# Performance work log

Measured on AMD Instinct MI355X. Metric: run time of the kernel, lower is better.

## Reference

```python
import jax, jax.numpy as jnp
import numpy as np

B, T, D, H, L = 2, 2048, 1024, 16, 12
DH = D // H


def setup_inputs() -> dict:
    key = jax.random.key(0)
    ks = jax.random.split(key, 12)
    s = 1.0 / np.sqrt(D)
    inp = {
        "x": jax.random.normal(ks[0], (B, T, D), dtype=jnp.float32),
        "Wq": jax.random.normal(ks[1], (D, D), dtype=jnp.float32) * s,
        "bq": jnp.zeros((D,), jnp.float32),
        "Wk": jax.random.normal(ks[2], (D, D), dtype=jnp.float32) * s,
        "bk": jnp.zeros((D,), jnp.float32),
        "Wv": jax.random.normal(ks[3], (D, D), dtype=jnp.float32) * s,
        "bv": jnp.zeros((D,), jnp.float32),
        "Wl": jax.random.normal(ks[4], (D, H * L), dtype=jnp.float32) * s,
        "bl": jnp.zeros((H * L,), jnp.float32),
        "Wo": jax.random.normal(ks[5], (D, D), dtype=jnp.float32) * s,
        "bo": jnp.zeros((D,), jnp.float32),
    }
    return inp


def _loglinear_scan(q, k, v, lam):
    # q,k,v: [B,T,H,DH]; lam: [B,T,H,L] (post-softplus gates per level)
    # Fenwick-tree (binary-counter) multi-level state; level L-1 is an
    # overflow sink so state size stays fixed at max_levels.
    qT = q.transpose(1, 0, 2, 3)      # [T,B,H,DH]
    kT = k.transpose(1, 0, 2, 3)
    vT = v.transpose(1, 0, 2, 3)
    lamT = lam.transpose(1, 0, 2, 3)  # [T,B,H,L]
    ts = jnp.arange(1, T + 1, dtype=jnp.int32)
    lev = jnp.arange(L)

    def step(S, inp):
        t, qt, kt, vt, lt = inp
        # j_raw = index of lowest set bit of t == trailing-ones(t-1)
        bits = jnp.right_shift(t, jnp.arange(32, dtype=jnp.int32)) & 1
        j_raw = jnp.argmax(bits).astype(jnp.int32)
        j = jnp.minimum(j_raw, L - 1)
        merge = (lev < j_raw)                              # [L] levels folded into j
        kv = kt[..., :, None] * vt[..., None, :]           # [B,H,DH,DH]
        merged = kv + jnp.einsum('l,bhlkv->bhkv', merge.astype(S.dtype), S)
        S = jnp.where(merge[None, None, :, None, None], 0.0, S)
        S = S.at[:, :, j].set(merged)
        # level-gated readout (includes current token, causal)
        ot = jnp.einsum('bhl,bhk,bhlkv->bhv', lt, qt, S)
        return S, ot

    S0 = jnp.zeros((B, H, L, DH, DH), q.dtype)
    _, o = jax.lax.scan(step, S0, (ts, qT, kT, vT, lamT))
    return o.transpose(1, 0, 2, 3)  # [B,T,H,DH]


def reference(x, Wq, bq, Wk, bk, Wv, bv, Wl, bl, Wo, bo):
    q = (x @ Wq + bq).reshape(B, T, H, DH)
    k = (x @ Wk + bk).reshape(B, T, H, DH)
    v = (x @ Wv + bv).reshape(B, T, H, DH)
    lam = jax.nn.softplus(x @ Wl + bl).reshape(B, T, H, L)
    y = _loglinear_scan(q, k, v, lam)
    return y.reshape(B, T, D) @ Wo + bo
```

## Files before the change

### kernel.cpp

```cpp
#include <hip/hip_runtime.h>

#define TT 2048
#define DD 1024
#define MTOT 4096

typedef float f32x4  __attribute__((ext_vector_type(4)));
typedef float f32x16 __attribute__((ext_vector_type(16)));

__device__ __forceinline__ unsigned short f2bf(float f) {
  union { float f; unsigned u; } c; c.f = f;
  return (unsigned short)((c.u + 0x7fffu + ((c.u >> 16) & 1u)) >> 16);
}

__device__ __forceinline__ void mfma16(f32x4& d, f32x4 a, f32x4 b) {
  asm volatile("v_mfma_f32_16x16x32_bf16 %0, %1, %2, %0" : "+v"(d) : "v"(a), "v"(b));
}
__device__ __forceinline__ void mfma32(f32x16& d, f32x4 a, f32x4 b) {
  asm volatile("v_mfma_f32_32x32x16_bf16 %0, %1, %2, %0" : "+v"(d) : "v"(a), "v"(b));
}
__device__ __forceinline__ float cvtpk(float lo, float hi) {
  float r;
  asm("v_cvt_pk_bf16_f32 %0, %1, %2" : "=v"(r) : "v"(lo), "v"(hi));
  return r;
}
__device__ __forceinline__ void plswap(float& a, float& b) {
  asm volatile("v_permlane32_swap_b32 %0, %1" : "+v"(a), "+v"(b));
}
__device__ __forceinline__ void gld16(void* lds, const void* g) {
  __builtin_amdgcn_global_load_lds(
      (const __attribute__((address_space(1))) unsigned int*)g,
      (__attribute__((address_space(3))) unsigned int*)lds, 16, 0, 0);
}
__device__ __forceinline__ void mfma_fence() {
  asm volatile("s_nop 7\n\ts_nop 7\n\ts_nop 7");
}
__device__ __forceinline__ void snop1() { asm volatile("s_nop 1"); }


__global__ void cast_x_kernel(const float* __restrict__ x, unsigned short* __restrict__ xbf) {
  int i = blockIdx.x * 256 + threadIdx.x;
  float4 v = ((const float4*)x)[i];
  ushort4 o; o.x = f2bf(v.x); o.y = f2bf(v.y); o.z = f2bf(v.z); o.w = f2bf(v.w);
  ((ushort4*)xbf)[i] = o;
}

__global__ void transpose_all(const float* __restrict__ Wq, const float* __restrict__ Wk,
                              const float* __restrict__ Wv, const float* __restrict__ Wl,
                              const float* __restrict__ Wo, unsigned short* __restrict__ Wcat) {
  __shared__ float tile[32][33];
  int n0 = blockIdx.x * 32, k0 = blockIdx.y * 32;
  int tx = threadIdx.x, ty = threadIdx.y;
  const float* src; int scol = 0, sN = 1024;
  if (n0 < 1024)      { src = Wq; scol = n0; }
  else if (n0 < 2048) { src = Wk; scol = n0 - 1024; }
  else if (n0 < 3072) { src = Wv; scol = n0 - 2048; }
  else if (n0 < 3264) { src = Wl; scol = n0 - 3072; sN = 192; }
  else if (n0 < 3328) { src = nullptr; }
  else                { src = Wo; scol = n0 - 3328; }
  if (src) {
#pragma unroll
    for (int i = 0; i < 4; ++i) tile[ty + i * 8][tx] = src[(k0 + ty + i * 8) * sN + scol + tx];
  }
  __syncthreads();
#pragma unroll
  for (int i = 0; i < 4; ++i)
    Wcat[(n0 + ty + i * 8) * 1024 + k0 + tx] = src ? f2bf(tile[tx][ty + i * 8]) : (unsigned short)0;
}

template <int BM, int MODE, int OCC>
__global__ __launch_bounds__(256, OCC) void gemm2(
    const unsigned short* __restrict__ A, const unsigned short* __restrict__ Bt,
    const float* __restrict__ b0p, const float* __restrict__ b1p,
    const float* __restrict__ b2p, const float* __restrict__ b3p,
    void* __restrict__ o0p, void* __restrict__ o1p, void* __restrict__ o2p, void* __restrict__ o3p) {
  constexpr int MF = BM / 32;
  __shared__ unsigned short As[BM * 64];
  __shared__ unsigned short Bs[128 * 64];
  const int tid = threadIdx.x;
  const int wid = tid >> 6, lane = tid & 63, l16 = lane & 15, g = lane >> 4;
  const int wm = wid >> 1, wn = wid & 1;
  const int m0 = blockIdx.y * BM, n0 = blockIdx.x * 128;
  const int rowlane = lane >> 3;
  const int swz = (lane & 7) ^ rowlane;

  f32x4 acc[MF][4] = {};

  for (int kb = 0; kb < 16; ++kb) {
    __syncthreads();
#pragma unroll
    for (int i = 0; i < MF; ++i) {
      int c = wid * MF + i;
      int row = c * 8 + rowlane;
      gld16((char*)As + c * 1024, A + (size_t)(m0 + row) * 1024 + kb * 64 + swz * 8);
    }
#pragma unroll
    for (int i = 0; i < 4; ++i) {
      int c = wid * 4 + i;
      int row = c * 8 + rowlane;
      gld16((char*)Bs + c * 1024, Bt + (size_t)(n0 + row) * 1024 + kb * 64 + swz * 8);
    }
    __syncthreads();
#pragma unroll
    for (int kk = 0; kk < 2; ++kk) {
      f32x4 a[MF], b[4];
#pragma unroll
      for (int f = 0; f < MF; ++f) {
        int ra = wm * (BM / 2) + f * 16 + l16;
        a[f] = *(const f32x4*)((const char*)As + ra * 128 + (((kk * 4 + g) ^ (ra & 7)) << 4));
      }
#pragma unroll
      for (int f = 0; f < 4; ++f) {
        int rb = wn * 64 + f * 16 + l16;
        b[f] = *(const f32x4*)((const char*)Bs + rb * 128 + (((kk * 4 + g) ^ (rb & 7)) << 4));
      }
#pragma unroll
      for (int mf = 0; mf < MF; ++mf)
#pragma unroll
        for (int nf = 0; nf < 4; ++nf) mfma16(acc[mf][nf], a[mf], b[nf]);
    }
  }
  mfma_fence();

#pragma unroll
  for (int nf = 0; nf < 4; ++nf) {
    int n = n0 + wn * 64 + nf * 16 + l16;
#pragma unroll
    for (int mf = 0; mf < MF; ++mf) {
      int m = m0 + wm * (BM / 2) + mf * 16 + g * 4;
      int bb = m >> 11, t = m & 2047;
      f32x4 v = acc[mf][nf];
      if (MODE == 1) {
        float bv = b0p[n];
        float* dst = (float*)o0p + ((size_t)m << 10) + n;
#pragma unroll
        for (int r = 0; r < 4; ++r) dst[(size_t)r << 10] = v[r] + bv;
      } else {
        int seg = n >> 10;
        int np = n & 1023;
        if (seg <= 1) {
          float bv = seg == 0 ? b0p[np] : b1p[np];
          unsigned short* dst = (unsigned short*)(seg == 0 ? o0p : o1p) +
              ((size_t)((bb << 4) + (np >> 6)) * TT + t) * 64 + (np & 63);
#pragma unroll
          for (int r = 0; r < 4; ++r) dst[r * 64] = f2bf(v[r] + bv);
        } else if (seg == 2) {
          float bv = b2p[np];
          ushort4 pk;
          pk.x = f2bf(v[0] + bv); pk.y = f2bf(v[1] + bv);
          pk.z = f2bf(v[2] + bv); pk.w = f2bf(v[3] + bv);
          *(ushort4*)((unsigned short*)o2p +
              ((size_t)((bb << 4) + (np >> 6)) * 64 + (np & 63)) * TT + t) = pk;
        } else if (np < 192) {
          float bv = b3p[np];
          int h = np / 12, l = np - h * 12;
          float* dst = (float*)o3p + ((size_t)((bb << 4) + h) * TT + t) * 12 + l;
#pragma unroll
          for (int r = 0; r < 4; ++r) {
            float s = v[r] + bv;
            dst[r * 12] = fmaxf(s, 0.f) + log1pf(expf(-fabsf(s)));
          }
        }
      }
    }
  }
}

__global__ __launch_bounds__(256, 2) void attn_fenwick2(
    const unsigned short* __restrict__ Qp, const unsigned short* __restrict__ Kp,
    const unsigned short* __restrict__ Vt, const float* __restrict__ lamp,
    unsigned short* __restrict__ Y) {
  __shared__ unsigned short Ks[2][64 * 128];
  __shared__ unsigned short Vs[2][64 * 128];
  __shared__ float laml[12 * 128];

  const int tid = threadIdx.x;
  const int w = tid >> 6, lane = tid & 63;
  const int q5 = lane & 31, hi = lane >> 5;

  int bx = blockIdx.x;
  int bh, jq;
  if (bx < 256) { bh = bx >> 4; jq = bx & 15; }
  else          { bh = 16 + ((bx - 256) >> 4); jq = 15 - (bx & 15); }

  const int qloc = w * 32 + q5;
  const int tqg = jq * 128 + qloc;

  {
    const float* src = lamp + ((size_t)bh * TT + jq * 128) * 12;
    for (int i = tid; i < 1536; i += 256) {
      int q = i / 12, l = i - q * 12;
      laml[l * 128 + q] = src[i];
    }
  }

  f32x4 qf[4];
  {
    const unsigned short* Qrow = Qp + ((size_t)bh * TT + tqg) * 64;
#pragma unroll
    for (int ks = 0; ks < 4; ++ks) qf[ks] = *(const f32x4*)(Qrow + ks * 16 + hi * 8);
  }

  f32x16 o0 = (f32x16)0.f, o1 = (f32x16)0.f;

  const unsigned short* Kbh = Kp + (size_t)bh * (TT * 64);
  const unsigned short* Vbh = Vt + (size_t)bh * (64 * TT);

  auto stage = [&](int kb, int buf) {
#pragma unroll
    for (int i = 0; i < 4; ++i) {
      int ch = w * 4 + i;
      int o = ch * 1024 + lane * 16;
      int r = o >> 8;
      int cp = (o >> 4) & 15;
      {
        int c = cp ^ (r & 15);
        gld16((char*)&Ks[buf][0] + ch * 1024,
              Kbh + (size_t)(kb * 128 + (c >> 3) * 64 + r) * 64 + (c & 7) * 8);
      }
      {
        int c = cp ^ (r & 15);
        gld16((char*)&Vs[buf][0] + ch * 1024,
              Vbh + (size_t)r * TT + kb * 128 + c * 8);
      }
    }
  };

  stage(0, 0);
  int cur = 0;

  for (int kb = 0; kb <= jq; ++kb) {
    __syncthreads();
    if (kb < jq) stage(kb + 1, cur ^ 1);
    const char* Kbase = (const char*)&Ks[cur][0];
    const char* Vbase = (const char*)&Vs[cur][0];
    const bool diag = (kb == jq);
    const int ntiles = diag ? (w + 1) : 4;

    f32x16 s[4];
#pragma unroll
    for (int t = 0; t < 4; ++t) {
      if (t >= ntiles) continue;
      s[t] = (f32x16)0.f;
      int r = (t & 1) * 32 + q5;
      int h = t >> 1;
#pragma unroll
      for (int ks = 0; ks < 4; ++ks) {
        int c = h * 8 + ks * 2 + hi;
        f32x4 kf = *(const f32x4*)(Kbase + r * 256 + ((c ^ (r & 15)) << 4));
        mfma32(s[t], kf, qf[ks]);
      }
    }
    mfma_fence();

#pragma unroll
    for (int t = 0; t < 4; ++t) {
      if (t >= ntiles) continue;
      int key64 = (kb << 1) + (t >> 1);
      float pkv[8];
      if (!diag || ((t >> 1) != (w >> 1))) {
        int lvl = 37 - __clz(((tqg + 1) >> 6) ^ key64);
        float wv = laml[lvl * 128 + qloc];
#pragma unroll
        for (int i = 0; i < 8; ++i)
          pkv[i] = cvtpk(s[t][2 * i] * wv, s[t][2 * i + 1] * wv);
      } else {
#pragma unroll
        for (int i = 0; i < 8; ++i) {
          float pe[2];
#pragma unroll
          for (int e = 0; e < 2; ++e) {
            int reg = 2 * i + e;
            int tig = kb * 128 + t * 32 + (reg & 3) + 8 * (reg >> 2) + 4 * hi;
            float pv = 0.f;
            if (tig <= tqg) {
              int lvl = 31 - __clz((tqg + 1) ^ tig);
              pv = s[t][reg] * laml[lvl * 128 + qloc];
            }
            pe[e] = pv;
          }
          pkv[i] = cvtpk(pe[0], pe[1]);
        }
      }
      plswap(pkv[0], pkv[2]);
      plswap(pkv[1], pkv[3]);
      plswap(pkv[4], pkv[6]);
      plswap(pkv[5], pkv[7]);
      f32x4 f0 = {pkv[0], pkv[1], pkv[2], pkv[3]};
      f32x4 f1 = {pkv[4], pkv[5], pkv[6], pkv[7]};
      snop1();
      int s0c = 4 * t + hi;
#pragma unroll
      for (int dg = 0; dg < 2; ++dg) {
        int row = dg * 32 + q5;
        f32x4 v0 = *(const f32x4*)(Vbase + row * 256 + ((s0c ^ (row & 15)) << 4));
        f32x4 v1 = *(const f32x4*)(Vbase + row * 256 + (((s0c + 2) ^ (row & 15)) << 4));
        if (dg) { mfma32(o1, v0, f0); mfma32(o1, v1, f1); }
        else    { mfma32(o0, v0, f0); mfma32(o0, v1, f1); }
      }
    }
    cur ^= 1;
  }
  mfma_fence();

  int b = bh >> 4, h = bh & 15;
  unsigned short* yrow = Y + ((size_t)(b * TT + tqg)) * DD + h * 64;
#pragma unroll
  for (int dg = 0; dg < 2; ++dg) {
    f32x16 o = dg ? o1 : o0;
#pragma unroll
    for (int rq = 0; rq < 4; ++rq) {
      ushort4 pk;
      pk.x = f2bf(o[4 * rq + 0]); pk.y = f2bf(o[4 * rq + 1]);
      pk.z = f2bf(o[4 * rq + 2]); pk.w = f2bf(o[4 * rq + 3]);
      *(ushort4*)(yrow + dg * 32 + 8 * rq + 4 * hi) = pk;
    }
  }
}


extern "C" void kernel_launch(void* const* d_in, const int* in_sizes, int n_in,
                              void* d_out, int out_size, void* d_ws, size_t ws_size,
                              hipStream_t stream) {
  const float* x  = (const float*)d_in[0];
  const float* Wq = (const float*)d_in[1];
  const float* bq = (const float*)d_in[2];
  const float* Wk = (const float*)d_in[3];
  const float* bk = (const float*)d_in[4];
  const float* Wv = (const float*)d_in[5];
  const float* bv = (const float*)d_in[6];
  const float* Wl = (const float*)d_in[7];
  const float* bl = (const float*)d_in[8];
  const float* Wo = (const float*)d_in[9];
  const float* bo = (const float*)d_in[10];

  char* ws = (char*)d_ws;
  size_t off = 0;
  auto alloc = [&](size_t bytes) { char* p = ws + off; off += bytes; return p; };

  unsigned short* xbf  = (unsigned short*)alloc((size_t)MTOT * DD * 2);
  unsigned short* Wcat = (unsigned short*)alloc((size_t)4352 * DD * 2);
  unsigned short* Qp   = (unsigned short*)alloc((size_t)MTOT * DD * 2);
  unsigned short* Kp   = (unsigned short*)alloc((size_t)MTOT * DD * 2);
  unsigned short* Vtb  = (unsigned short*)alloc((size_t)MTOT * DD * 2);
  float*          lamp = (float*)alloc((size_t)32 * TT * 12 * 4);
  unsigned short* Y    = (unsigned short*)alloc((size_t)MTOT * DD * 2);
  (void)ws_size; (void)off; (void)in_sizes; (void)n_in; (void)out_size;

  cast_x_kernel<<<MTOT * DD / 4 / 256, 256, 0, stream>>>(x, xbf);
  transpose_all<<<dim3(136, 32), dim3(32, 8), 0, stream>>>(Wq, Wk, Wv, Wl, Wo, Wcat);

  gemm2<128, 0, 4><<<dim3(26, 32), 256, 0, stream>>>(
      xbf, Wcat, bq, bk, bv, bl, Qp, Kp, Vtb, lamp);

  attn_fenwick2<<<dim3(512), 256, 0, stream>>>(Qp, Kp, Vtb, lamp, Y);

  gemm2<64, 1, 6><<<dim3(8, 64), 256, 0, stream>>>(
      Y, Wcat + (size_t)3328 * 1024, bo, nullptr, nullptr, nullptr,
      (float*)d_out, nullptr, nullptr, nullptr);
}
```

Before: 131.5 us.

## Double-buffer GEMM staging and pair causal query tiles per attention block

The GEMM kernels now double-buffer the A/B LDS tiles so the next k-block loads while MFMAs run on the current one. The output GEMM is fixed at 128-row tiles, giving fewer, larger blocks. The attention kernel now pairs a short query tile j with its mirror 15-j in one block, so each staged K/V tile is reused by both and per-block work is balanced. That gives 256 blocks at occupancy 1, trading parallelism and extra registers and LDS for better reuse and load balance.

```diff
diff --git a/kernel.cpp b/kernel.cpp
--- a/kernel.cpp
+++ b/kernel.cpp
@@ -67,57 +67,54 @@
     Wcat[(n0 + ty + i * 8) * 1024 + k0 + tx] = src ? f2bf(tile[tx][ty + i * 8]) : (unsigned short)0;
 }
 
-template <int BM, int MODE, int OCC>
-__global__ __launch_bounds__(256, OCC) void gemm2(
+template <int MODE>
+__device__ __forceinline__ void gemm_body(
     const unsigned short* __restrict__ A, const unsigned short* __restrict__ Bt,
     const float* __restrict__ b0p, const float* __restrict__ b1p,
     const float* __restrict__ b2p, const float* __restrict__ b3p,
     void* __restrict__ o0p, void* __restrict__ o1p, void* __restrict__ o2p, void* __restrict__ o3p) {
-  constexpr int MF = BM / 32;
-  __shared__ unsigned short As[BM * 64];
-  __shared__ unsigned short Bs[128 * 64];
+  __shared__ unsigned short As[2][128 * 64];
+  __shared__ unsigned short Bs[2][128 * 64];
   const int tid = threadIdx.x;
   const int wid = tid >> 6, lane = tid & 63, l16 = lane & 15, g = lane >> 4;
   const int wm = wid >> 1, wn = wid & 1;
-  const int m0 = blockIdx.y * BM, n0 = blockIdx.x * 128;
+  const int m0 = blockIdx.y * 128, n0 = blockIdx.x * 128;
   const int rowlane = lane >> 3;
   const int swz = (lane & 7) ^ rowlane;
 
-  f32x4 acc[MF][4] = {};
-
-  for (int kb = 0; kb < 16; ++kb) {
-    __syncthreads();
-#pragma unroll
-    for (int i = 0; i < MF; ++i) {
-      int c = wid * MF + i;
-      int row = c * 8 + rowlane;
-      gld16((char*)As + c * 1024, A + (size_t)(m0 + row) * 1024 + kb * 64 + swz * 8);
-    }
+  f32x4 acc[4][4] = {};
+
+  auto stage = [&](int kb, int buf) {
 #pragma unroll
     for (int i = 0; i < 4; ++i) {
       int c = wid * 4 + i;
       int row = c * 8 + rowlane;
-      gld16((char*)Bs + c * 1024, Bt + (size_t)(n0 + row) * 1024 + kb * 64 + swz * 8);
-    }
+      gld16((char*)&As[buf][0] + c * 1024, A + (size_t)(m0 + row) * 1024 + kb * 64 + swz * 8);
+      gld16((char*)&Bs[buf][0] + c * 1024, Bt + (size_t)(n0 + row) * 1024 + kb * 64 + swz * 8);
+    }
+  };
+
+  stage(0, 0);
+  int cur = 0;
+  for (int kb = 0; kb < 16; ++kb) {
     __syncthreads();
+    if (kb < 15) stage(kb + 1, cur ^ 1);
 #pragma unroll
     for (int kk = 0; kk < 2; ++kk) {
-      f32x4 a[MF], b[4];
-#pragma unroll
-      for (int f = 0; f < MF; ++f) {
-        int ra = wm * (BM / 2) + f * 16 + l16;
-        a[f] = *(const f32x4*)((const char*)As + ra * 128 + (((kk * 4 + g) ^ (ra & 7)) << 4));
-      }
+      f32x4 a[4], b[4];
 #pragma unroll
       for (int f = 0; f < 4; ++f) {
+        int ra = wm * 64 + f * 16 + l16;
+        a[f] = *(const f32x4*)((const char*)&As[cur][0] + ra * 128 + (((kk * 4 + g) ^ (ra & 7)) << 4));
         int rb = wn * 64 + f * 16 + l16;
-        b[f] = *(const f32x4*)((const char*)Bs + rb * 128 + (((kk * 4 + g) ^ (rb & 7)) << 4));
-      }
-#pragma unroll
-      for (int mf = 0; mf < MF; ++mf)
+        b[f] = *(const f32x4*)((const char*)&Bs[cur][0] + rb * 128 + (((kk * 4 + g) ^ (rb & 7)) << 4));
+      }
+#pragma unroll
+      for (int mf = 0; mf < 4; ++mf)
 #pragma unroll
         for (int nf = 0; nf < 4; ++nf) mfma16(acc[mf][nf], a[mf], b[nf]);
     }
+    cur ^= 1;
   }
   mfma_fence();
 
@@ -125,8 +122,8 @@
   for (int nf = 0; nf < 4; ++nf) {
     int n = n0 + wn * 64 + nf * 16 + l16;
 #pragma unroll
-    for (int mf = 0; mf < MF; ++mf) {
-      int m = m0 + wm * (BM / 2) + mf * 16 + g * 4;
+    for (int mf = 0; mf < 4; ++mf) {
+      int m = m0 + wm * 64 + mf * 16 + g * 4;
       int bb = m >> 11, t = m & 2047;
       f32x4 v = acc[mf][nf];
       if (MODE == 1) {
@@ -165,42 +162,63 @@
   }
 }
 
-__global__ __launch_bounds__(256, 2) void attn_fenwick2(
+__global__ __launch_bounds__(256, 2) void gemm_qkvl(
+    const unsigned short* __restrict__ A, const unsigned short* __restrict__ Bt,
+    const float* b0, const float* b1, const float* b2, const float* b3,
+    void* o0, void* o1, void* o2, void* o3) {
+  gemm_body<0>(A, Bt, b0, b1, b2, b3, o0, o1, o2, o3);
+}
+
+__global__ __launch_bounds__(256, 2) void gemm_out(
+    const unsigned short* __restrict__ A, const unsigned short* __restrict__ Bt,
+    const float* b0, void* o0) {
+  gemm_body<1>(A, Bt, b0, nullptr, nullptr, nullptr, o0, nullptr, nullptr, nullptr);
+}
+
+__global__ __launch_bounds__(256, 1) void attn_fenwick3(
     const unsigned short* __restrict__ Qp, const unsigned short* __restrict__ Kp,
     const unsigned short* __restrict__ Vt, const float* __restrict__ lamp,
     unsigned short* __restrict__ Y) {
   __shared__ unsigned short Ks[2][64 * 128];
   __shared__ unsigned short Vs[2][64 * 128];
-  __shared__ float laml[12 * 128];
+  __shared__ float lamlA[12 * 128];
+  __shared__ float lamlB[12 * 128];
 
   const int tid = threadIdx.x;
   const int w = tid >> 6, lane = tid & 63;
   const int q5 = lane & 31, hi = lane >> 5;
 
-  int bx = blockIdx.x;
-  int bh, jq;
-  if (bx < 256) { bh = bx >> 4; jq = bx & 15; }
-  else          { bh = 16 + ((bx - 256) >> 4); jq = 15 - (bx & 15); }
+  const int bx = blockIdx.x;
+  const int bh = bx >> 3, j = bx & 7;
+  const int jA = j, jB = 15 - j;
 
   const int qloc = w * 32 + q5;
-  const int tqg = jq * 128 + qloc;
+  const int tqA = jA * 128 + qloc;
+  const int tqB = jB * 128 + qloc;
 
   {
-    const float* src = lamp + ((size_t)bh * TT + jq * 128) * 12;
+    const float* srcA = lamp + ((size_t)bh * TT + jA * 128) * 12;
+    const float* srcB = lamp + ((size_t)bh * TT + jB * 128) * 12;
     for (int i = tid; i < 1536; i += 256) {
       int q = i / 12, l = i - q * 12;
-      laml[l * 128 + q] = src[i];
-    }
-  }
-
-  f32x4 qf[4];
+      lamlA[l * 128 + q] = srcA[i];
+      lamlB[l * 128 + q] = srcB[i];
+    }
+  }
+
+  f32x4 qfA[4], qfB[4];
   {
-    const unsigned short* Qrow = Qp + ((size_t)bh * TT + tqg) * 64;
-#pragma unroll
-    for (int ks = 0; ks < 4; ++ks) qf[ks] = *(const f32x4*)(Qrow + ks * 16 + hi * 8);
-  }
-
-  f32x16 o0 = (f32x16)0.f, o1 = (f32x16)0.f;
+    const unsigned short* QrA = Qp + ((size_t)bh * TT + tqA) * 64;
+    const unsigned short* QrB = Qp + ((size_t)bh * TT + tqB) * 64;
+#pragma unroll
+    for (int ks = 0; ks < 4; ++ks) {
+      qfA[ks] = *(const f32x4*)(QrA + ks * 16 + hi * 8);
+      qfB[ks] = *(const f32x4*)(QrB + ks * 16 + hi * 8);
+    }
+  }
+
+  f32x16 oA0 = (f32x16)0.f, oA1 = (f32x16)0.f;
+  f32x16 oB0 = (f32x16)0.f, oB1 = (f32x16)0.f;
 
   const unsigned short* Kbh = Kp + (size_t)bh * (TT * 64);
   const unsigned short* Vbh = Vt + (size_t)bh * (64 * TT);
@@ -212,28 +230,18 @@
       int o = ch * 1024 + lane * 16;
       int r = o >> 8;
       int cp = (o >> 4) & 15;
-      {
-        int c = cp ^ (r & 15);
-        gld16((char*)&Ks[buf][0] + ch * 1024,
-              Kbh + (size_t)(kb * 128 + (c >> 3) * 64 + r) * 64 + (c & 7) * 8);
-      }
-      {
-        int c = cp ^ (r & 15);
-        gld16((char*)&Vs[buf][0] + ch * 1024,
-              Vbh + (size_t)r * TT + kb * 128 + c * 8);
-      }
+      int c = cp ^ (r & 15);
+      gld16((char*)&Ks[buf][0] + ch * 1024,
+            Kbh + (size_t)(kb * 128 + (c >> 3) * 64 + r) * 64 + (c & 7) * 8);
+      gld16((char*)&Vs[buf][0] + ch * 1024,
+            Vbh + (size_t)r * TT + kb * 128 + c * 8);
     }
   };
 
-  stage(0, 0);
-  int cur = 0;
-
-  for (int kb = 0; kb <= jq; ++kb) {
-    __syncthreads();
-    if (kb < jq) stage(kb + 1, cur ^ 1);
+  auto do_tile = [&](int kb, int cur, int tqg, const float* laml, const f32x4* qf,
+                     f32x16& o0, f32x16& o1, bool diag) {
     const char* Kbase = (const char*)&Ks[cur][0];
     const char* Vbase = (const char*)&Vs[cur][0];
-    const bool diag = (kb == jq);
     const int ntiles = diag ? (w + 1) : 4;
 
     f32x16 s[4];
@@ -298,21 +306,36 @@
         else    { mfma32(o0, v0, f0); mfma32(o0, v1, f1); }
       }
     }
+  };
+
+  stage(0, 0);
+  int cur = 0;
+
+  for (int kb = 0; kb <= jB; ++kb) {
+    __syncthreads();
+    if (kb < jB) stage(kb + 1, cur ^ 1);
+    do_tile(kb, cur, tqB, lamlB, qfB, oB0, oB1, kb == jB);
+    if (kb <= jA) do_tile(kb, cur, tqA, lamlA, qfA, oA0, oA1, kb == jA);
     cur ^= 1;
   }
   mfma_fence();
 
   int b = bh >> 4, h = bh & 15;
-  unsigned short* yrow = Y + ((size_t)(b * TT + tqg)) * DD + h * 64;
+  unsigned short* yA = Y + ((size_t)(b * TT + tqA)) * DD + h * 64;
+  unsigned short* yB = Y + ((size_t)(b * TT + tqB)) * DD + h * 64;
 #pragma unroll
   for (int dg = 0; dg < 2; ++dg) {
-    f32x16 o = dg ? o1 : o0;
+    f32x16 oa = dg ? oA1 : oA0;
+    f32x16 ob = dg ? oB1 : oB0;
 #pragma unroll
     for (int rq = 0; rq < 4; ++rq) {
-      ushort4 pk;
-      pk.x = f2bf(o[4 * rq + 0]); pk.y = f2bf(o[4 * rq + 1]);
-      pk.z = f2bf(o[4 * rq + 2]); pk.w = f2bf(o[4 * rq + 3]);
-      *(ushort4*)(yrow + dg * 32 + 8 * rq + 4 * hi) = pk;
+      ushort4 pa, pb;
+      pa.x = f2bf(oa[4 * rq + 0]); pa.y = f2bf(oa[4 * rq + 1]);
+      pa.z = f2bf(oa[4 * rq + 2]); pa.w = f2bf(oa[4 * rq + 3]);
+      pb.x = f2bf(ob[4 * rq + 0]); pb.y = f2bf(ob[4 * rq + 1]);
+      pb.z = f2bf(ob[4 * rq + 2]); pb.w = f2bf(ob[4 * rq + 3]);
+      *(ushort4*)(yA + dg * 32 + 8 * rq + 4 * hi) = pa;
+      *(ushort4*)(yB + dg * 32 + 8 * rq + 4 * hi) = pb;
     }
   }
 }
@@ -349,12 +372,11 @@
   cast_x_kernel<<<MTOT * DD / 4 / 256, 256, 0, stream>>>(x, xbf);
   transpose_all<<<dim3(136, 32), dim3(32, 8), 0, stream>>>(Wq, Wk, Wv, Wl, Wo, Wcat);
 
-  gemm2<128, 0, 4><<<dim3(26, 32), 256, 0, stream>>>(
+  gemm_qkvl<<<dim3(26, 32), 256, 0, stream>>>(
       xbf, Wcat, bq, bk, bv, bl, Qp, Kp, Vtb, lamp);
 
-  attn_fenwick2<<<dim3(512), 256, 0, stream>>>(Qp, Kp, Vtb, lamp, Y);
-
-  gemm2<64, 1, 6><<<dim3(8, 64), 256, 0, stream>>>(
-      Y, Wcat + (size_t)3328 * 1024, bo, nullptr, nullptr, nullptr,
-      (float*)d_out, nullptr, nullptr, nullptr);
-}
+  attn_fenwick3<<<dim3(256), 256, 0, stream>>>(Qp, Kp, Vtb, lamp, Y);
+
+  gemm_out<<<dim3(8, 32), 256, 0, stream>>>(
+      Y, Wcat + (size_t)3328 * 1024, bo, (float*)d_out);
+}
```

New measurement: 140.1 us. 6.6% more time.
